# Performance work log

Measured on AMD Instinct MI355X. Metric: run time of the kernel, lower is better.

The kernel has to match this reference:

```python
import jax, jax.numpy as jnp
import numpy as np

NQ, NH = 7, 4          # quantiles x horizons
G = NQ * NH            # 28 independent branches
IN_DIM, H1, H2 = 64, 64, 32


def setup_inputs() -> dict:
    key = jax.random.key(0)
    ks = jax.random.split(key, 7)
    B = 131072
    x = jax.random.normal(ks[0], (B, IN_DIM), dtype=jnp.float32)
    s1 = 1.0 / np.sqrt(IN_DIM)
    s2 = 1.0 / np.sqrt(H1)
    s3 = 1.0 / np.sqrt(H2)
    W1 = jax.random.uniform(ks[1], (G, IN_DIM, H1), jnp.float32, -s1, s1)
    b1 = jax.random.uniform(ks[2], (G, H1), jnp.float32, -s1, s1)
    W2 = jax.random.uniform(ks[3], (G, H1, H2), jnp.float32, -s2, s2)
    b2 = jax.random.uniform(ks[4], (G, H2), jnp.float32, -s2, s2)
    W3 = jax.random.uniform(ks[5], (G, H2, 1), jnp.float32, -s3, s3)
    b3 = jax.random.uniform(ks[6], (G, 1), jnp.float32, -s3, s3)
    return {"x": x, "W1": W1, "b1": b1, "W2": W2, "b2": b2, "W3": W3, "b3": b3}


def reference(x, W1, b1, W2, b2, W3, b3):
    # All G branches fused as batched GEMMs. x: [B, in]
    B = x.shape[0]
    h = jax.nn.relu(jnp.einsum('bi,gij->gbj', x, W1) + b1[:, None, :])   # [G,B,H1]
    h = jax.nn.relu(jnp.einsum('gbj,gjk->gbk', h, W2) + b2[:, None, :])  # [G,B,H2]
    o = jnp.einsum('gbk,gko->gbo', h, W3) + b3[:, None, :]               # [G,B,1]
    # branch order matches nested loop: quantile outer, horizon inner
    out = o[..., 0].reshape(NQ, NH, B).transpose(2, 0, 1)                # [B,NQ,NH]
    return out
```

## Files before the change

### kernel.cpp

```cpp
#include <hip/hip_runtime.h>
#include <hip/hip_bf16.h>
#include <hip/hip_fp16.h>

#define GN 28
#define G_TILE_BYTES 12288
#define WS_BYTES (GN * G_TILE_BYTES)

typedef __attribute__((ext_vector_type(4))) float f32x4;
typedef __attribute__((ext_vector_type(8))) short short8;
typedef _Float16 f16x8 __attribute__((ext_vector_type(8)));

__device__ __forceinline__ unsigned short f2h(float v){
  __half h = __float2half(v);
  return __builtin_bit_cast(unsigned short, h);
}
__device__ __forceinline__ f32x4 mfma16f(short8 a, short8 b, f32x4 c){
  return __builtin_amdgcn_mfma_f32_16x16x32_f16(
      __builtin_bit_cast(f16x8, a), __builtin_bit_cast(f16x8, b), c, 0, 0, 0);
}

__global__ __launch_bounds__(256) void prep_weights(
    const float* __restrict__ W1, const float* __restrict__ W2,
    unsigned char* __restrict__ ws){
  __shared__ float t1[64*65];
  __shared__ float t2[64*33];
  const int g = blockIdx.x;
  const int tid = threadIdx.x;

  {
    const f32x4* src = (const f32x4*)(W1 + g*4096);
    int k = tid >> 2, n0 = (tid & 3) * 16;
    #pragma unroll
    for (int j = 0; j < 4; ++j){
      f32x4 v = src[tid*4 + j];
      #pragma unroll
      for (int e = 0; e < 4; ++e) t1[k*65 + n0 + j*4 + e] = v[e];
    }
  }
  {
    const f32x4* src = (const f32x4*)(W2 + g*2048);
    int k = tid >> 2, n0 = (tid & 3) * 8;
    #pragma unroll
    for (int j = 0; j < 2; ++j){
      f32x4 v = src[tid*2 + j];
      #pragma unroll
      for (int e = 0; e < 4; ++e) t2[k*33 + n0 + j*4 + e] = v[e];
    }
  }
  __syncthreads();

  unsigned char* base = ws + g*G_TILE_BYTES;
  {
    int n = tid & 63, mh = tid >> 6;
    #pragma unroll
    for (int h = 0; h < 2; ++h){
      unsigned w[4];
      #pragma unroll
      for (int mm = 0; mm < 4; ++mm){
        int m = mh*8 + h*4 + mm;
        float lo = t1[(2*m    )*65 + n];
        float hi = t1[(2*m + 1)*65 + n];
        w[mm] = (unsigned)f2h(lo) | ((unsigned)f2h(hi) << 16);
      }
      int off = (n*128 + mh*32 + h*16) ^ ((n & 7) << 4);
      *(uint4*)(base + off) = make_uint4(w[0], w[1], w[2], w[3]);
    }
  }
  {
    int n2 = tid & 31, mq = tid >> 5;
    unsigned w[4];
    #pragma unroll
    for (int mm = 0; mm < 4; ++mm){
      int m = mq*4 + mm;
      int kk = 2*m;
      int ks = kk >> 5, qq = (kk >> 3) & 3, u = (kk >> 2) & 1, i = kk & 3;
      int kn = 32*ks + 16*u + 4*qq + i;
      float lo = t2[(kn    )*33 + n2];
      float hi = t2[(kn + 1)*33 + n2];
      w[mm] = (unsigned)f2h(lo) | ((unsigned)f2h(hi) << 16);
    }
    int off = (n2*128 + mq*16) ^ ((n2 & 7) << 4);
    *(uint4*)(base + 8192 + off) = make_uint4(w[0], w[1], w[2], w[3]);
  }
}

__global__ __launch_bounds__(128, 2) void mlp_fused(
    const float* __restrict__ x,  const float* __restrict__ b1,
    const float* __restrict__ b2, const float* __restrict__ W3,
    const float* __restrict__ b3, const unsigned char* __restrict__ ws,
    float* __restrict__ out){
  __shared__ uint4 wbuf[2][768];

  const int tid = threadIdx.x;
  const int wv  = tid >> 6;
  const int ln  = tid & 63;
  const int l15 = ln & 15;
  const int q   = ln >> 4;
  const int rowBase = blockIdx.x * 128 + wv * 64;

  short8 xf[4][2];
  #pragma unroll
  for (int rt = 0; rt < 4; ++rt)
    #pragma unroll
    for (int ks = 0; ks < 2; ++ks){
      const float* p = x + (rowBase + rt*16 + l15)*64 + ks*32 + q*8;
      f32x4 a = *(const f32x4*)p;
      f32x4 b = *(const f32x4*)(p + 4);
      short8 s;
      #pragma unroll
      for (int j = 0; j < 4; ++j){
        s[j]   = (short)f2h(a[j]);
        s[4+j] = (short)f2h(b[j]);
      }
      xf[rt][ks] = s;
    }

  auto stage = [&](int g, int buf){
    const unsigned char* gb = ws + g*G_TILE_BYTES + wv*6144 + ln*16;
    uint4* lb = &wbuf[buf][wv*384];
    #pragma unroll
    for (int it = 0; it < 6; ++it){
      __builtin_amdgcn_global_load_lds(
          (const __attribute__((address_space(1))) void*)(gb + it*1024),
          (__attribute__((address_space(3))) void*)(lb + it*64), 16, 0, 0);
    }
  };

  stage(0, 0);
  asm volatile("s_waitcnt vmcnt(0)" ::: "memory");
  __syncthreads();

  const f32x4 z4 = {0.f, 0.f, 0.f, 0.f};

  for (int g = 0; g < GN; ++g){
    const int cur = g & 1;
    if (g + 1 < GN) stage(g + 1, cur ^ 1);
    const uint4* wb = wbuf[cur];

    f32x4 bias1v[4], bias2v[2], w3v[2];
    #pragma unroll
    for (int nt = 0; nt < 4; ++nt)
      bias1v[nt] = *(const f32x4*)(b1 + g*64 + nt*16 + q*4);
    #pragma unroll
    for (int nt = 0; nt < 2; ++nt){
      bias2v[nt] = *(const f32x4*)(b2 + g*32 + nt*16 + q*4);
      w3v[nt]    = *(const f32x4*)(W3 + g*32 + nt*16 + q*4);
    }
    float bias3 = b3[g];

    short8 a1[4][2];
    #pragma unroll
    for (int nt = 0; nt < 4; ++nt)
      #pragma unroll
      for (int ks = 0; ks < 2; ++ks){
        int n = nt*16 + l15;
        int off = ((n*128 + ks*64 + q*16) ^ ((n & 7) << 4)) >> 4;
        a1[nt][ks] = __builtin_bit_cast(short8, wb[off]);
      }
    f32x4 acc1[4][4];
    #pragma unroll
    for (int nt = 0; nt < 4; ++nt)
      #pragma unroll
      for (int rt = 0; rt < 4; ++rt){
        acc1[nt][rt] = mfma16f(a1[nt][0], xf[rt][0], z4);
        acc1[nt][rt] = mfma16f(a1[nt][1], xf[rt][1], acc1[nt][rt]);
      }

    short8 bh[4][2];
    #pragma unroll
    for (int rt = 0; rt < 4; ++rt)
      #pragma unroll
      for (int ks = 0; ks < 2; ++ks){
        f32x4 v0 = acc1[2*ks][rt]     + bias1v[2*ks];
        f32x4 v1 = acc1[2*ks + 1][rt] + bias1v[2*ks + 1];
        short8 h;
        #pragma unroll
        for (int i = 0; i < 4; ++i){
          h[i]   = (short)f2h(fmaxf(v0[i], 0.0f));
          h[4+i] = (short)f2h(fmaxf(v1[i], 0.0f));
        }
        bh[rt][ks] = h;
      }

    short8 a2[2][2];
    #pragma unroll
    for (int nt = 0; nt < 2; ++nt)
      #pragma unroll
      for (int ks = 0; ks < 2; ++ks){
        int n2 = nt*16 + l15;
        int off = ((n2*128 + ks*64 + q*16) ^ ((n2 & 7) << 4)) >> 4;
        a2[nt][ks] = __builtin_bit_cast(short8, wb[512 + off]);
      }
    f32x4 acc2[2][4];
    #pragma unroll
    for (int nt = 0; nt < 2; ++nt)
      #pragma unroll
      for (int rt = 0; rt < 4; ++rt){
        acc2[nt][rt] = mfma16f(a2[nt][0], bh[rt][0], z4);
        acc2[nt][rt] = mfma16f(a2[nt][1], bh[rt][1], acc2[nt][rt]);
      }

    #pragma unroll
    for (int rt = 0; rt < 4; ++rt){
      float p = 0.0f;
      #pragma unroll
      for (int nt = 0; nt < 2; ++nt){
        f32x4 v = acc2[nt][rt] + bias2v[nt];
        #pragma unroll
        for (int i = 0; i < 4; ++i)
          p = fmaf(fmaxf(v[i], 0.0f), w3v[nt][i], p);
      }
      p += __shfl_xor(p, 16);
      p += __shfl_xor(p, 32);
      p += bias3;
      if (ln < 16)
        out[(rowBase + rt*16 + ln)*28 + g] = p;
    }

    asm volatile("s_waitcnt vmcnt(0)" ::: "memory");
    __syncthreads();
  }
}

extern "C" void kernel_launch(void* const* d_in, const int* in_sizes, int n_in,
                              void* d_out, int out_size, void* d_ws, size_t ws_size,
                              hipStream_t stream){
  const float* x  = (const float*)d_in[0];
  const float* W1 = (const float*)d_in[1];
  const float* b1 = (const float*)d_in[2];
  const float* W2 = (const float*)d_in[3];
  const float* b2 = (const float*)d_in[4];
  const float* W3 = (const float*)d_in[5];
  const float* b3 = (const float*)d_in[6];
  unsigned char* ws = (unsigned char*)d_ws;
  float* out = (float*)d_out;
  if (ws_size < (size_t)WS_BYTES) return;
  hipLaunchKernelGGL(prep_weights, dim3(GN), dim3(256), 0, stream, W1, W2, ws);
  hipLaunchKernelGGL(mlp_fused, dim3(1024), dim3(128), 0, stream,
                     x, b1, b2, W3, b3, ws, out);
}
```

Measured before the change: 153.1 us.

## Software-pipeline layer-1 MFMAs of next branch with layer-2 of current branch

```diff
diff --git a/kernel.cpp b/kernel.cpp
--- a/kernel.cpp
+++ b/kernel.cpp
@@ -9,6 +9,7 @@
 typedef __attribute__((ext_vector_type(4))) float f32x4;
 typedef __attribute__((ext_vector_type(8))) short short8;
 typedef _Float16 f16x8 __attribute__((ext_vector_type(8)));
+typedef __fp16 pk16x2 __attribute__((ext_vector_type(2)));
 
 __device__ __forceinline__ unsigned short f2h(float v){
   __half h = __float2half(v);
@@ -89,7 +90,7 @@
     const float* __restrict__ b2, const float* __restrict__ W3,
     const float* __restrict__ b3, const unsigned char* __restrict__ ws,
     float* __restrict__ out){
-  __shared__ uint4 wbuf[2][768];
+  __shared__ uint4 wbuf[3][768];
 
   const int tid = threadIdx.x;
   const int wv  = tid >> 6;
@@ -115,6 +116,22 @@
       xf[rt][ks] = s;
     }
 
+  int offA1[4][2], offA2[2][2];
+  #pragma unroll
+  for (int nt = 0; nt < 4; ++nt)
+    #pragma unroll
+    for (int ks = 0; ks < 2; ++ks){
+      int n = nt*16 + l15;
+      offA1[nt][ks] = ((n*128 + ks*64 + q*16) ^ ((n & 7) << 4)) >> 4;
+    }
+  #pragma unroll
+  for (int nt = 0; nt < 2; ++nt)
+    #pragma unroll
+    for (int ks = 0; ks < 2; ++ks){
+      int n2 = nt*16 + l15;
+      offA2[nt][ks] = (((n2*128 + ks*64 + q*16) ^ ((n2 & 7) << 4)) >> 4) + 512;
+    }
+
   auto stage = [&](int g, int buf){
     const unsigned char* gb = ws + g*G_TILE_BYTES + wv*6144 + ln*16;
     uint4* lb = &wbuf[buf][wv*384];
@@ -126,90 +143,108 @@
     }
   };
 
+  auto packrelu = [&](const f32x4& v0, const f32x4& v1) -> short8 {
+    union { unsigned u[4]; short8 s; } r;
+    pk16x2 t0 = __builtin_amdgcn_cvt_pkrtz(fmaxf(v0[0],0.f), fmaxf(v0[1],0.f));
+    pk16x2 t1 = __builtin_amdgcn_cvt_pkrtz(fmaxf(v0[2],0.f), fmaxf(v0[3],0.f));
+    pk16x2 t2 = __builtin_amdgcn_cvt_pkrtz(fmaxf(v1[0],0.f), fmaxf(v1[1],0.f));
+    pk16x2 t3 = __builtin_amdgcn_cvt_pkrtz(fmaxf(v1[2],0.f), fmaxf(v1[3],0.f));
+    r.u[0] = __builtin_bit_cast(unsigned, t0);
+    r.u[1] = __builtin_bit_cast(unsigned, t1);
+    r.u[2] = __builtin_bit_cast(unsigned, t2);
+    r.u[3] = __builtin_bit_cast(unsigned, t3);
+    return r.s;
+  };
+
+  f32x4 accA[4][4], accB[4][4];
+
   stage(0, 0);
+  f32x4 b1c[4];
+  #pragma unroll
+  for (int nt = 0; nt < 4; ++nt)
+    b1c[nt] = *(const f32x4*)(b1 + 0*64 + nt*16 + q*4);
   asm volatile("s_waitcnt vmcnt(0)" ::: "memory");
   __syncthreads();
-
-  const f32x4 z4 = {0.f, 0.f, 0.f, 0.f};
-
-  for (int g = 0; g < GN; ++g){
-    const int cur = g & 1;
-    if (g + 1 < GN) stage(g + 1, cur ^ 1);
-    const uint4* wb = wbuf[cur];
-
-    f32x4 bias1v[4], bias2v[2], w3v[2];
-    #pragma unroll
-    for (int nt = 0; nt < 4; ++nt)
-      bias1v[nt] = *(const f32x4*)(b1 + g*64 + nt*16 + q*4);
+  stage(1, 1);
+  {
+    short8 a1f[4][2];
+    #pragma unroll
+    for (int nt = 0; nt < 4; ++nt)
+      #pragma unroll
+      for (int ks = 0; ks < 2; ++ks)
+        a1f[nt][ks] = __builtin_bit_cast(short8, wbuf[0][offA1[nt][ks]]);
+    #pragma unroll
+    for (int nt = 0; nt < 4; ++nt)
+      #pragma unroll
+      for (int rt = 0; rt < 4; ++rt){
+        accA[nt][rt] = mfma16f(a1f[nt][0], xf[rt][0], b1c[nt]);
+        accA[nt][rt] = mfma16f(a1f[nt][1], xf[rt][1], accA[nt][rt]);
+      }
+  }
+  asm volatile("s_waitcnt vmcnt(0)" ::: "memory");
+  __syncthreads();
+
+  auto body = [&](int g, f32x4 (&accC)[4][4], f32x4 (&accN)[4][4]){
+    const int gn = (g + 1 < GN) ? g + 1 : GN - 1;
+    if (g + 2 < GN) stage(g + 2, (g + 2) % 3);
+    const uint4* wbN = wbuf[gn % 3];
+    const uint4* wbC = wbuf[g % 3];
+
+    f32x4 b1N[4];
+    #pragma unroll
+    for (int nt = 0; nt < 4; ++nt)
+      b1N[nt] = *(const f32x4*)(b1 + gn*64 + nt*16 + q*4);
+    short8 a1n[4][2];
+    #pragma unroll
+    for (int nt = 0; nt < 4; ++nt)
+      #pragma unroll
+      for (int ks = 0; ks < 2; ++ks)
+        a1n[nt][ks] = __builtin_bit_cast(short8, wbN[offA1[nt][ks]]);
+    #pragma unroll
+    for (int nt = 0; nt < 4; ++nt)
+      #pragma unroll
+      for (int rt = 0; rt < 4; ++rt){
+        accN[nt][rt] = mfma16f(a1n[nt][0], xf[rt][0], b1N[nt]);
+        accN[nt][rt] = mfma16f(a1n[nt][1], xf[rt][1], accN[nt][rt]);
+      }
+
+    short8 bh[4][2];
+    #pragma unroll
+    for (int rt = 0; rt < 4; ++rt)
+      #pragma unroll
+      for (int ks = 0; ks < 2; ++ks)
+        bh[rt][ks] = packrelu(accC[2*ks][rt], accC[2*ks + 1][rt]);
+
+    f32x4 b2v[2], w3v[2];
     #pragma unroll
     for (int nt = 0; nt < 2; ++nt){
-      bias2v[nt] = *(const f32x4*)(b2 + g*32 + nt*16 + q*4);
-      w3v[nt]    = *(const f32x4*)(W3 + g*32 + nt*16 + q*4);
-    }
+      b2v[nt] = *(const f32x4*)(b2 + g*32 + nt*16 + q*4);
+      w3v[nt] = *(const f32x4*)(W3 + g*32 + nt*16 + q*4);
+    }
+    short8 a2[2][2];
+    #pragma unroll
+    for (int nt = 0; nt < 2; ++nt)
+      #pragma unroll
+      for (int ks = 0; ks < 2; ++ks)
+        a2[nt][ks] = __builtin_bit_cast(short8, wbC[offA2[nt][ks]]);
+    f32x4 acc2[2][4];
+    #pragma unroll
+    for (int nt = 0; nt < 2; ++nt)
+      #pragma unroll
+      for (int rt = 0; rt < 4; ++rt){
+        acc2[nt][rt] = mfma16f(a2[nt][0], bh[rt][0], b2v[nt]);
+        acc2[nt][rt] = mfma16f(a2[nt][1], bh[rt][1], acc2[nt][rt]);
+      }
+
     float bias3 = b3[g];
-
-    short8 a1[4][2];
-    #pragma unroll
-    for (int nt = 0; nt < 4; ++nt)
-      #pragma unroll
-      for (int ks = 0; ks < 2; ++ks){
-        int n = nt*16 + l15;
-        int off = ((n*128 + ks*64 + q*16) ^ ((n & 7) << 4)) >> 4;
-        a1[nt][ks] = __builtin_bit_cast(short8, wb[off]);
-      }
-    f32x4 acc1[4][4];
-    #pragma unroll
-    for (int nt = 0; nt < 4; ++nt)
-      #pragma unroll
-      for (int rt = 0; rt < 4; ++rt){
-        acc1[nt][rt] = mfma16f(a1[nt][0], xf[rt][0], z4);
-        acc1[nt][rt] = mfma16f(a1[nt][1], xf[rt][1], acc1[nt][rt]);
-      }
-
-    short8 bh[4][2];
-    #pragma unroll
-    for (int rt = 0; rt < 4; ++rt)
-      #pragma unroll
-      for (int ks = 0; ks < 2; ++ks){
-        f32x4 v0 = acc1[2*ks][rt]     + bias1v[2*ks];
-        f32x4 v1 = acc1[2*ks + 1][rt] + bias1v[2*ks + 1];
-        short8 h;
-        #pragma unroll
-        for (int i = 0; i < 4; ++i){
-          h[i]   = (short)f2h(fmaxf(v0[i], 0.0f));
-          h[4+i] = (short)f2h(fmaxf(v1[i], 0.0f));
-        }
-        bh[rt][ks] = h;
-      }
-
-    short8 a2[2][2];
-    #pragma unroll
-    for (int nt = 0; nt < 2; ++nt)
-      #pragma unroll
-      for (int ks = 0; ks < 2; ++ks){
-        int n2 = nt*16 + l15;
-        int off = ((n2*128 + ks*64 + q*16) ^ ((n2 & 7) << 4)) >> 4;
-        a2[nt][ks] = __builtin_bit_cast(short8, wb[512 + off]);
-      }
-    f32x4 acc2[2][4];
-    #pragma unroll
-    for (int nt = 0; nt < 2; ++nt)
-      #pragma unroll
-      for (int rt = 0; rt < 4; ++rt){
-        acc2[nt][rt] = mfma16f(a2[nt][0], bh[rt][0], z4);
-        acc2[nt][rt] = mfma16f(a2[nt][1], bh[rt][1], acc2[nt][rt]);
-      }
-
     #pragma unroll
     for (int rt = 0; rt < 4; ++rt){
       float p = 0.0f;
       #pragma unroll
-      for (int nt = 0; nt < 2; ++nt){
-        f32x4 v = acc2[nt][rt] + bias2v[nt];
+      for (int nt = 0; nt < 2; ++nt)
         #pragma unroll
         for (int i = 0; i < 4; ++i)
-          p = fmaf(fmaxf(v[i], 0.0f), w3v[nt][i], p);
-      }
+          p = fmaf(fmaxf(acc2[nt][rt][i], 0.0f), w3v[nt][i], p);
       p += __shfl_xor(p, 16);
       p += __shfl_xor(p, 32);
       p += bias3;
@@ -219,6 +254,11 @@
 
     asm volatile("s_waitcnt vmcnt(0)" ::: "memory");
     __syncthreads();
+  };
+
+  for (int gg = 0; gg < GN; gg += 2){
+    body(gg,     accA, accB);
+    body(gg + 1, accB, accA);
   }
 }
 
```

After: 151.3 us. Within noise of the previous version (-1.1%).
